# Kernel tuning notes

Measured on AMD Instinct MI355X. Metric: run time of the kernel, lower is better.

The kernel has to match this reference:

```python
import jax, jax.numpy as jnp
import numpy as np

N = 32768      # nodes
H = 128        # hidden_channels
G = 50         # num_gaussians
F = 128        # num_filters
E = 524288     # edges (avg degree 16)
CUTOFF = 10.0
LOG2 = np.float32(np.log(2.0))


def _lin_init(key, fan_in, fan_out):
    return (jax.random.normal(key, (fan_in, fan_out), jnp.float32) / jnp.sqrt(jnp.float32(fan_in)))


def setup_inputs() -> dict:
    key = jax.random.key(0)
    ks = jax.random.split(key, 12)
    h = jax.random.normal(ks[0], (N, H), jnp.float32)
    pos = jax.random.uniform(ks[1], (N, 3), jnp.float32, minval=0.0, maxval=10.0)
    edge_index = jax.random.randint(ks[2], (2, E), 0, N, jnp.int32)
    virtual_edge_mask = jax.random.randint(ks[3], (E,), 0, 2, jnp.int32) == 1
    return {
        "h": h, "pos": pos,
        "edge_index": edge_index, "virtual_edge_mask": virtual_edge_mask,
        # attn_mlp: Linear(2H+G, H) -> ReLU -> Linear(H, 1)
        "attn_w1": _lin_init(ks[4], 2 * H + G, H), "attn_b1": jnp.zeros((H,), jnp.float32),
        "attn_w2": _lin_init(ks[5], H, 1), "attn_b2": jnp.zeros((1,), jnp.float32),
        # CFConv filter mlp: Linear(G, F) -> ssp -> Linear(F, F)
        "filt_w1": _lin_init(ks[6], G, F), "filt_b1": jnp.zeros((F,), jnp.float32),
        "filt_w2": _lin_init(ks[7], F, F), "filt_b2": jnp.zeros((F,), jnp.float32),
        # CFConv lin1 (no bias), lin2; InteractionBlock output lin
        "lin1_w": _lin_init(ks[8], H, F),
        "lin2_w": _lin_init(ks[9], F, H), "lin2_b": jnp.zeros((H,), jnp.float32),
        "lin_w": _lin_init(ks[10], H, H), "lin_b": jnp.zeros((H,), jnp.float32),
    }


def _ssp(x):  # ShiftedSoftplus
    return jax.nn.softplus(x) - LOG2


def _gaussian_smearing(d):  # [E] -> [E, G]
    offset = jnp.linspace(0.0, CUTOFF, G, dtype=jnp.float32)
    coeff = -0.5 / (offset[1] - offset[0]) ** 2
    return jnp.exp(coeff * (d[:, None] - offset) ** 2)


def _masked_scatter_softmax(score, seg, mask):
    # softmax of score over edges grouped by seg, restricted to mask; 1.0 elsewhere
    neg = jnp.where(mask, score, -jnp.inf)
    m = jax.ops.segment_max(neg, seg, num_segments=N)
    m = jnp.where(jnp.isfinite(m), m, 0.0)
    e = jnp.where(mask, jnp.exp(score - m[seg]), 0.0)
    s = jax.ops.segment_sum(e, seg, num_segments=N)
    return jnp.where(mask, e / (s[seg] + 1e-16), 1.0)


def reference(h, pos, edge_index, virtual_edge_mask,
              attn_w1, attn_b1, attn_w2, attn_b2,
              filt_w1, filt_b1, filt_w2, filt_b2,
              lin1_w, lin2_w, lin2_b, lin_w, lin_b):
    row, col = edge_index[0], edge_index[1]
    d = jnp.linalg.norm(pos[row] - pos[col], axis=-1)          # [E]
    edge_attr = _gaussian_smearing(d)                          # [E, G]

    # attention score over cat(h_i, h_j, edge_attr)
    feat = jnp.concatenate([h[row], h[col], edge_attr], axis=-1)   # [E, 2H+G]
    score = (jax.nn.relu(feat @ attn_w1 + attn_b1) @ attn_w2 + attn_b2)[:, 0]  # [E]
    decay = _masked_scatter_softmax(score, row, virtual_edge_mask)  # [E]
    edge_attr = edge_attr * decay[:, None]

    # PyG SchNet InteractionBlock / CFConv
    C = 0.5 * (jnp.cos(d * jnp.float32(np.pi) / CUTOFF) + 1.0)     # [E]
    W = (_ssp(edge_attr @ filt_w1 + filt_b1) @ filt_w2 + filt_b2) * C[:, None]  # [E, F]
    x = h @ lin1_w                                                  # [N, F]
    msg = x[row] * W                                                # [E, F]
    agg = jax.ops.segment_sum(msg, col, num_segments=N)             # [N, F]
    x = agg @ lin2_w + lin2_b
    h_update = _ssp(x) @ lin_w + lin_b                              # [N, H]
    return h_update, pos
```

## Files before the change

kernel.cpp:

```cpp
#include <hip/hip_runtime.h>

#define NN 32768
#define HH 128
#define GG 50
#define EE 524288
#define TBINS 8192

constexpr float GSTEP = 10.0f / 49.0f;
constexpr float GCOEF = -0.5f / (GSTEP * GSTEP);
constexpr float PI_OVER_CUT = 0.31415926535897931f;
constexpr float LOG2F_ = 0.69314718055994531f;
constexpr float LOG2E_ = 1.4426950408889634f;
constexpr float RLOG2E_ = 0.69314718055994531f;
constexpr float GC2 = GCOEF * LOG2E_;
constexpr float DMAX_ = 17.4f;
constexpr float BIN_SCALE = (float)TBINS / DMAX_;
constexpr float BIN_INV   = DMAX_ / (float)TBINS;

typedef __attribute__((ext_vector_type(8))) short bf16x8;
typedef __attribute__((ext_vector_type(4))) float f32x4;
typedef unsigned short ushort_t;

__device__ __forceinline__ float fast_exp2(float x) {
    float r; asm("v_exp_f32 %0, %1" : "=v"(r) : "v"(x)); return r;
}
__device__ __forceinline__ float fast_log2(float x) {
    float r; asm("v_log_f32 %0, %1" : "=v"(r) : "v"(x)); return r;
}
__device__ __forceinline__ float fexpf(float x) {
    return fast_exp2(x * LOG2E_);
}
__device__ __forceinline__ float sspf(float x) {
    const float p = fast_exp2(x * LOG2E_);
    const float r = RLOG2E_ * fast_log2(1.0f + p) - LOG2F_;
    return (x > 80.0f) ? (x - LOG2F_) : r;
}
__device__ __forceinline__ unsigned fenc(float f) {
    unsigned b = __float_as_uint(f);
    return (b & 0x80000000u) ? ~b : (b | 0x80000000u);
}
__device__ __forceinline__ float fdec(unsigned u) {
    unsigned b = (u & 0x80000000u) ? (u ^ 0x80000000u) : ~u;
    return __uint_as_float(b);
}
__device__ __forceinline__ int get_mask(const void* mp, int mode, int e) {
    if (mode) return ((const unsigned char*)mp)[e] != 0;
    return ((const int*)mp)[e] != 0;
}
__device__ __forceinline__ ushort_t f2bf(float f) {
    unsigned u = __float_as_uint(f);
    return (ushort_t)((u + 0x7FFFu + ((u >> 16) & 1u)) >> 16);
}
__device__ __forceinline__ float bf2f(ushort_t s) { return __uint_as_float(((unsigned)s) << 16); }

__global__ void k_detect(const unsigned char* __restrict__ mb, int* __restrict__ flag) {
    __shared__ int any;
    if (threadIdx.x == 0) any = 0;
    __syncthreads();
    int local = 0;
    for (int i = threadIdx.x; i < 16384; i += blockDim.x)
        if ((i & 3) != 0 && mb[i]) local = 1;
    if (local) atomicOr(&any, 1);
    __syncthreads();
    if (threadIdx.x == 0) *flag = any;
}

__global__ void k_prep_w(const float* __restrict__ filt_w2,
                         const float* __restrict__ attn_w1, const float* __restrict__ lin1_w,
                         const float* __restrict__ lin2_w, const float* __restrict__ lin_w,
                         ushort_t* __restrict__ w2t, ushort_t* __restrict__ wut,
                         ushort_t* __restrict__ wvt, ushort_t* __restrict__ wxt,
                         ushort_t* __restrict__ l2t, ushort_t* __restrict__ lwt)
{
    const int t = blockIdx.x * 256 + threadIdx.x;
    if (t < 16384) {
        const int n = t >> 7, k = t & 127;
        w2t[t] = f2bf(filt_w2[k * HH + n]);
    } else if (t < 32768) {
        const int i = t - 16384, n = i >> 7, k = i & 127;
        wut[i] = f2bf(attn_w1[(size_t)k * HH + n]);
    } else if (t < 49152) {
        const int i = t - 32768, n = i >> 7, k = i & 127;
        wvt[i] = f2bf(attn_w1[(size_t)(128 + k) * HH + n]);
    } else if (t < 65536) {
        const int i = t - 49152, n = i >> 7, k = i & 127;
        wxt[i] = f2bf(lin1_w[(size_t)k * HH + n]);
    } else if (t < 81920) {
        const int i = t - 65536, n = i >> 7, k = i & 127;
        l2t[i] = f2bf(lin2_w[(size_t)k * HH + n]);
    } else if (t < 98304) {
        const int i = t - 81920, n = i >> 7, k = i & 127;
        lwt[i] = f2bf(lin_w[(size_t)k * HH + n]);
    }
}

__global__ __launch_bounds__(256) void k_prep_tab(
    const float* __restrict__ filt_w1, const float* __restrict__ attn_w1,
    const float* __restrict__ attn_b1,
    ushort_t* __restrict__ atab, ushort_t* __restrict__ btab)
{
    __shared__ float ga[2][GG];
    const int tid = threadIdx.x;
    const int half = tid >> 7, j = tid & 127;
    const int bin = blockIdx.x * 2 + half;
    const float d = bin * BIN_INV;
    if (j < GG) {
        const float t = d - j * GSTEP;
        ga[half][j] = fast_exp2(GC2 * t * t);
    }
    __syncthreads();
    float a = 0.0f, b = attn_b1[j];
    for (int g = 0; g < GG; g++) {
        const float gv = ga[half][g];
        a += gv * filt_w1[g * HH + j];
        b += gv * attn_w1[(size_t)(256 + g) * HH + j];
    }
    atab[(size_t)bin * HH + j] = f2bf(a);
    btab[(size_t)bin * HH + j] = f2bf(b);
}

__global__ __launch_bounds__(256, 4) void k_node_proj(
    const float* __restrict__ h,
    const ushort_t* __restrict__ wut, const ushort_t* __restrict__ wvt,
    const ushort_t* __restrict__ wxt,
    ushort_t* __restrict__ ub, ushort_t* __restrict__ vb, ushort_t* __restrict__ xhb)
{
    __shared__ alignas(16) unsigned char smem[32768];
    unsigned char* HB = smem;
    unsigned char* WB = smem + 16384;

    const int tid = threadIdx.x;
    const int n0 = blockIdx.x * 64;
    const int mat = blockIdx.y;
    const ushort_t* __restrict__ wt = (mat == 0) ? wut : (mat == 1 ? wvt : wxt);
    ushort_t* __restrict__ out = (mat == 0) ? ub : (mat == 1 ? vb : xhb);

    for (int p = tid; p < 2048; p += 256) {
        const int row = p >> 5, c4 = p & 31;
        const float4 v = *(const float4*)(h + (size_t)(n0 + row) * HH + c4 * 4);
        uint2 pk = {(unsigned)f2bf(v.x) | ((unsigned)f2bf(v.y) << 16),
                    (unsigned)f2bf(v.z) | ((unsigned)f2bf(v.w) << 16)};
        const int lbyte = row * 256 + c4 * 8;
        *(uint2*)(HB + (lbyte ^ ((row & 7) << 4))) = pk;
    }
    for (int p = tid; p < 1024; p += 256) {
        const int byte = p * 16; const int nl = byte >> 8;
        *(float4*)(WB + (byte ^ ((nl & 7) << 4))) = *(const float4*)((const char*)wt + byte);
    }
    __syncthreads();

    const int lane = tid & 63, wv = tid >> 6, col0 = lane & 15, g4 = lane >> 4;
    const int m = wv * 16 + col0;
    f32x4 acc[8] = {};
#pragma unroll
    for (int hh2 = 0; hh2 < 2; hh2++) {
        if (hh2 == 1) {
            __syncthreads();
            for (int p = tid; p < 1024; p += 256) {
                const int byte = p * 16; const int nl = byte >> 8;
                *(float4*)(WB + (byte ^ ((nl & 7) << 4))) =
                    *(const float4*)((const char*)wt + 16384 + byte);
            }
            __syncthreads();
        }
#pragma unroll
        for (int kk = 0; kk < 4; kk++) {
            const int abyte = m * 256 + kk * 64 + g4 * 16;
            const bf16x8 af = *(const bf16x8*)(HB + (abyte ^ ((m & 7) << 4)));
#pragma unroll
            for (int q = 0; q < 4; q++) {
                const int l = q * 16 + col0;
                const int bbyte = l * 256 + kk * 64 + g4 * 16;
                const bf16x8 bf_ = *(const bf16x8*)(WB + (bbyte ^ ((l & 7) << 4)));
                acc[hh2 * 4 + q] = __builtin_amdgcn_mfma_f32_16x16x32_bf16(af, bf_, acc[hh2 * 4 + q], 0, 0, 0);
            }
        }
    }
#pragma unroll
    for (int f = 0; f < 8; f++) {
        const int col = (f >> 2) * 64 + (f & 3) * 16 + col0;
#pragma unroll
        for (int rg = 0; rg < 4; rg++) {
            const int row = wv * 16 + g4 * 4 + rg;
            out[(size_t)(n0 + row) * HH + col] = f2bf(acc[f][rg]);
        }
    }
}

#define CPB 2048
__global__ __launch_bounds__(256) void k_compact(
    const int* __restrict__ ei, const void* __restrict__ maskp,
    const int* __restrict__ flagp,
    int* __restrict__ count, int* __restrict__ mcount,
    uint2* __restrict__ mrec)
{
    __shared__ uint2 buf[CPB];
    __shared__ int lcnt, gbase;
    const int tid = threadIdx.x;
    const int lane = tid & 63;
    if (tid == 0) lcnt = 0;
    __syncthreads();

    const int base = blockIdx.x * CPB;
    const int mode = *flagp;
#pragma unroll
    for (int i = 0; i < CPB; i += 256) {
        const int e = base + i + tid;
        const int r = ei[e], c = ei[EE + e];
        atomicAdd(&count[c], 1);
        const int msk = get_mask(maskp, mode, e);
        const unsigned long long ball = __ballot(msk);
        const int rank = __popcll(ball & ((1ull << lane) - 1ull));
        int wb = 0;
        if (lane == 0 && ball) wb = atomicAdd(&lcnt, __popcll(ball));
        wb = __shfl(wb, 0, 64);
        if (msk) {
            uint2 rec = {(unsigned)e, (unsigned)r | ((unsigned)c << 16)};
            buf[wb + rank] = rec;
        }
    }
    __syncthreads();
    if (tid == 0) gbase = atomicAdd(mcount, lcnt);
    __syncthreads();
    const int n = lcnt, gb = gbase;
    for (int i = tid; i < n; i += 256)
        mrec[gb + i] = buf[i];
}

__global__ __launch_bounds__(256, 8) void k_edge_score(
    const float* __restrict__ pos, const uint2* __restrict__ mrec,
    const int* __restrict__ mcount,
    const ushort_t* __restrict__ ub, const ushort_t* __restrict__ vb,
    const ushort_t* __restrict__ btab,
    const float* __restrict__ attn_w2, const float* __restrict__ attn_b2,
    float* __restrict__ score, unsigned* __restrict__ menc)
{
    __shared__ int rsh[64], csh[64], esh[64], bsh[64];
    __shared__ int Em_s;

    const int tid  = threadIdx.x;
    if (tid == 0) Em_s = *mcount;
    __syncthreads();
    const int Em = Em_s;
    const int base = blockIdx.x * 64;
    if (base >= Em) return;

    const int lane = tid & 63;
    const int wv   = tid >> 6;
    const int col0 = lane & 15;
    const int g4   = lane >> 4;

    if (tid < 64) {
        const int slot = base + tid;
        int e = -1, r = 0, c = 0;
        if (slot < Em) {
            const uint2 rec = mrec[slot];
            e = (int)rec.x;
            r = (int)(rec.y & 0xFFFFu);
            c = (int)(rec.y >> 16);
        }
        esh[tid] = e; rsh[tid] = r; csh[tid] = c;
        const float dx = pos[r * 3 + 0] - pos[c * 3 + 0];
        const float dy = pos[r * 3 + 1] - pos[c * 3 + 1];
        const float dz = pos[r * 3 + 2] - pos[c * 3 + 2];
        const float d = sqrtf(dx * dx + dy * dy + dz * dz);
        int bin = (int)(d * BIN_SCALE + 0.5f);
        bsh[tid] = (bin > TBINS - 1) ? TBINS - 1 : bin;
    }
    __syncthreads();

    const float4 w20 = *(const float4*)(attn_w2 + col0 * 8);
    const float4 w21 = *(const float4*)(attn_w2 + col0 * 8 + 4);
    const float w2v[8] = {w20.x, w20.y, w20.z, w20.w, w21.x, w21.y, w21.z, w21.w};

    float pe[4];
#pragma unroll
    for (int rg = 0; rg < 4; rg++) {
        const int le = wv * 16 + g4 * 4 + rg;
        const int r = rsh[le], c = csh[le], bin = bsh[le];
        const bf16x8 uu = *(const bf16x8*)(ub + (size_t)r * HH + col0 * 8);
        const bf16x8 vv = *(const bf16x8*)(vb + (size_t)c * HH + col0 * 8);
        const bf16x8 bb = *(const bf16x8*)(btab + (size_t)bin * HH + col0 * 8);
        float s = 0.0f;
#pragma unroll
        for (int b = 0; b < 8; b++) {
            float z = bf2f((ushort_t)uu[b]) + bf2f((ushort_t)vv[b]) + bf2f((ushort_t)bb[b]);
            z = fmaxf(z, 0.0f);
            s += z * w2v[b];
        }
        pe[rg] = s;
    }
#pragma unroll
    for (int mask = 1; mask <= 8; mask <<= 1) {
#pragma unroll
        for (int rg = 0; rg < 4; rg++)
            pe[rg] += __shfl_xor(pe[rg], mask, 64);
    }
    if (col0 == 0) {
        const float b2 = attn_b2[0];
#pragma unroll
        for (int rg = 0; rg < 4; rg++) {
            const int le = wv * 16 + g4 * 4 + rg;
            const int e = esh[le];
            if (e >= 0) {
                const float s = pe[rg] + b2;
                score[e] = s;
                atomicMax(&menc[rsh[le]], fenc(s));
            }
        }
    }
}

__global__ void k_ssum(const uint2* __restrict__ mrec, const int* __restrict__ mcount,
                       const float* __restrict__ score, const unsigned* __restrict__ menc,
                       float* __restrict__ ssum)
{
    const int slot = blockIdx.x * 256 + threadIdx.x;
    if (slot >= *mcount) return;
    const uint2 rec = mrec[slot];
    const int e = (int)rec.x;
    const int r = (int)(rec.y & 0xFFFFu);
    atomicAdd(&ssum[r], fexpf(score[e] - fdec(menc[r])));
}

__global__ __launch_bounds__(512) void k_scan(const int* __restrict__ count,
                                              int* __restrict__ cursor)
{
    __shared__ int s[512];
    const int t = threadIdx.x;
    const int base_i = t * 64;
    int sum = 0;
    for (int i = 0; i < 64; i++) sum += count[base_i + i];
    s[t] = sum;
    __syncthreads();
    for (int off = 1; off < 512; off <<= 1) {
        int v = (t >= off) ? s[t - off] : 0;
        __syncthreads();
        s[t] += v;
        __syncthreads();
    }
    int run = s[t] - sum;
    for (int i = 0; i < 64; i++) {
        cursor[base_i + i] = run;
        run += count[base_i + i];
    }
}

__global__ void k_scatter(const int* __restrict__ ei, const void* __restrict__ maskp,
                          const int* __restrict__ flagp, const float* __restrict__ pos,
                          const float* __restrict__ score,
                          const unsigned* __restrict__ menc, const float* __restrict__ ssum,
                          int* __restrict__ cursor, uint4* __restrict__ erec)
{
    const int e = blockIdx.x * 256 + threadIdx.x;
    if (e >= EE) return;
    const int r = ei[e], c = ei[EE + e];
    const int p = atomicAdd(&cursor[c], 1);
    const float dx = pos[r * 3 + 0] - pos[c * 3 + 0];
    const float dy = pos[r * 3 + 1] - pos[c * 3 + 1];
    const float dz = pos[r * 3 + 2] - pos[c * 3 + 2];
    const float d = sqrtf(dx * dx + dy * dy + dz * dz);
    int bin = (int)(d * BIN_SCALE + 0.5f);
    bin = (bin > TBINS - 1) ? TBINS - 1 : bin;
    float dec = 1.0f;
    const int mode = *flagp;
    if (get_mask(maskp, mode, e)) {
        const float m = fdec(menc[r]);
        dec = fexpf(score[e] - m) / (ssum[r] + 1e-16f);
    }
    uint4 rec = {__float_as_uint(d), __float_as_uint(dec),
                 (unsigned)r | ((unsigned)c << 16), (unsigned)bin};
    erec[p] = rec;
}

__global__ __launch_bounds__(256, 4) void k_filter_mfma(
    const uint4* __restrict__ erec,
    const ushort_t* __restrict__ atab, const float* __restrict__ filt_b1,
    const ushort_t* __restrict__ w2t, const float* __restrict__ filt_b2,
    const ushort_t* __restrict__ xhb, float* __restrict__ agg)
{
    __shared__ alignas(16) unsigned char smem[32768];
    unsigned char* T1 = smem;
    unsigned char* WB = smem + 16384;
    float* msgb = (float*)smem;

    __shared__ float decsh[64], Csh[64];
    __shared__ int rsh[64], csh[64], bsh[64];
    __shared__ int shflags;

    const int tid  = threadIdx.x;
    const int e0   = blockIdx.x * 64;
    const int lane = tid & 63;
    const int wv   = tid >> 6;
    const int col0 = lane & 15;
    const int g4   = lane >> 4;

    if (tid < 64) {
        const uint4 rec = erec[e0 + tid];
        const float d = __uint_as_float(rec.x);
        decsh[tid] = __uint_as_float(rec.y);
        rsh[tid] = (int)(rec.z & 0xFFFFu);
        csh[tid] = (int)(rec.z >> 16);
        bsh[tid] = (int)rec.w;
        Csh[tid] = 0.5f * (cosf(d * PI_OVER_CUT) + 1.0f);
    }
    if (tid == 64) {
        const unsigned cf = erec[e0].z >> 16;
        const unsigned cl = erec[e0 + 63].z >> 16;
        int f = 0;
        if (e0 > 0 && (erec[e0 - 1].z >> 16) == cf) f |= 1;
        if (e0 + 64 < EE && (erec[e0 + 64].z >> 16) == cl) f |= 2;
        shflags = f;
    }
    for (int p = tid; p < 1024; p += 256) {
        const int byte = p * 16; const int nl = byte >> 8;
        *(float4*)(WB + (byte ^ ((nl & 7) << 4))) = *(const float4*)((const char*)w2t + byte);
    }
    __syncthreads();

    {
        const int e = tid & 63, q = tid >> 6;
        const float dec = decsh[e];
        const ushort_t* arow = atab + (size_t)bsh[e] * HH;
#pragma unroll
        for (int c8 = 0; c8 < 4; c8++) {
            const int col = q * 32 + c8 * 8;
            const bf16x8 av = *(const bf16x8*)(arow + col);
            const float4 fb0 = *(const float4*)(filt_b1 + col);
            const float4 fb1 = *(const float4*)(filt_b1 + col + 4);
            const float bb[8] = {fb0.x, fb0.y, fb0.z, fb0.w, fb1.x, fb1.y, fb1.z, fb1.w};
            bf16x8 pk;
#pragma unroll
            for (int b = 0; b < 8; b++)
                pk[b] = (short)f2bf(sspf(dec * bf2f((ushort_t)av[b]) + bb[b]));
            const int lbyte = e * 256 + col * 2;
            *(bf16x8*)(T1 + (lbyte ^ ((e & 7) << 4))) = pk;
        }
    }
    int rr[4]; float CC[4];
#pragma unroll
    for (int rg = 0; rg < 4; rg++) {
        const int e = wv * 16 + g4 * 4 + rg;
        rr[rg] = rsh[e];
        CC[rg] = Csh[e];
    }
    ushort_t xr[4][8];
#pragma unroll
    for (int rg = 0; rg < 4; rg++)
#pragma unroll
        for (int n = 0; n < 8; n++)
            xr[rg][n] = xhb[(size_t)rr[rg] * HH + n * 16 + col0];
    float b2v[8];
#pragma unroll
    for (int n = 0; n < 8; n++)
        b2v[n] = filt_b2[n * 16 + col0];
    __syncthreads();

    const int m = wv * 16 + col0;
    f32x4 acc2[8] = {};
#pragma unroll
    for (int kk = 0; kk < 4; kk++) {
        const int abyte = m * 256 + kk * 64 + g4 * 16;
        const bf16x8 af = *(const bf16x8*)(T1 + (abyte ^ ((m & 7) << 4)));
#pragma unroll
        for (int q = 0; q < 4; q++) {
            const int l = q * 16 + col0;
            const int bbyte = l * 256 + kk * 64 + g4 * 16;
            const bf16x8 bf_ = *(const bf16x8*)(WB + (bbyte ^ ((l & 7) << 4)));
            acc2[q] = __builtin_amdgcn_mfma_f32_16x16x32_bf16(af, bf_, acc2[q], 0, 0, 0);
        }
    }
    __syncthreads();
    for (int p = tid; p < 1024; p += 256) {
        const int byte = p * 16; const int nl = byte >> 8;
        *(float4*)(WB + (byte ^ ((nl & 7) << 4))) =
            *(const float4*)((const char*)w2t + 16384 + byte);
    }
    __syncthreads();
#pragma unroll
    for (int kk = 0; kk < 4; kk++) {
        const int abyte = m * 256 + kk * 64 + g4 * 16;
        const bf16x8 af = *(const bf16x8*)(T1 + (abyte ^ ((m & 7) << 4)));
#pragma unroll
        for (int q = 0; q < 4; q++) {
            const int l = q * 16 + col0;
            const int bbyte = l * 256 + kk * 64 + g4 * 16;
            const bf16x8 bf_ = *(const bf16x8*)(WB + (bbyte ^ ((l & 7) << 4)));
            acc2[4 + q] = __builtin_amdgcn_mfma_f32_16x16x32_bf16(af, bf_, acc2[4 + q], 0, 0, 0);
        }
    }
    __syncthreads();

#pragma unroll
    for (int n = 0; n < 8; n++) {
        const int col = n * 16 + col0;
#pragma unroll
        for (int rg = 0; rg < 4; rg++) {
            const int e = wv * 16 + g4 * 4 + rg;
            const float Wv = (acc2[n][rg] + b2v[n]) * CC[rg];
            const float xv = __uint_as_float(((unsigned)xr[rg][n]) << 16);
            msgb[e * 128 + ((col + 8 * g4) & 127)] = xv * Wv;
        }
    }
    __syncthreads();

    {
        const int q = tid >> 7;
        const int j = tid & 127;
        const int base = q * 32;
        const int fl = shflags;
        const int cfirst = csh[base], clast = csh[base + 31];
        const int f1 = (q == 0) ? (fl & 1) : (csh[base - 1] == cfirst);
        const int f2 = (q == 1) ? (fl & 2) : (csh[base + 32] == clast);
        float a = msgb[base * 128 + ((j + 8 * ((base >> 2) & 3)) & 127)];
        int cur = cfirst;
        for (int e = base + 1; e < base + 32; e++) {
            const int de = csh[e];
            if (de != cur) {
                if ((cur == cfirst && f1) || (cur == clast && f2))
                    atomicAdd(&agg[(size_t)cur * HH + j], a);
                else
                    agg[(size_t)cur * HH + j] = a;
                a = 0.0f;
                cur = de;
            }
            a += msgb[e * 128 + ((j + 8 * ((e >> 2) & 3)) & 127)];
        }
        if ((cur == cfirst && f1) || (cur == clast && f2))
            atomicAdd(&agg[(size_t)cur * HH + j], a);
        else
            agg[(size_t)cur * HH + j] = a;
    }
}

__global__ __launch_bounds__(256, 4) void k_final(
    const float* __restrict__ agg, const ushort_t* __restrict__ l2t,
    const float* __restrict__ lin2_b, const ushort_t* __restrict__ lwt,
    const float* __restrict__ lin_b, float* __restrict__ out)
{
    __shared__ alignas(16) unsigned char smem[32768];
    unsigned char* AB = smem;
    unsigned char* WB = smem + 16384;
    unsigned char* T1 = smem;

    const int tid = threadIdx.x;
    const int n0 = blockIdx.x * 64;

    for (int p = tid; p < 2048; p += 256) {
        const int row = p >> 5, c4 = p & 31;
        const float4 v = *(const float4*)(agg + (size_t)(n0 + row) * HH + c4 * 4);
        uint2 pk = {(unsigned)f2bf(v.x) | ((unsigned)f2bf(v.y) << 16),
                    (unsigned)f2bf(v.z) | ((unsigned)f2bf(v.w) << 16)};
        const int lbyte = row * 256 + c4 * 8;
        *(uint2*)(AB + (lbyte ^ ((row & 7) << 4))) = pk;
    }
    for (int p = tid; p < 1024; p += 256) {
        const int byte = p * 16; const int nl = byte >> 8;
        *(float4*)(WB + (byte ^ ((nl & 7) << 4))) = *(const float4*)((const char*)l2t + byte);
    }
    __syncthreads();

    const int lane = tid & 63, wv = tid >> 6, col0 = lane & 15, g4 = lane >> 4;
    const int m = wv * 16 + col0;
    float b1v[8], b2v[8];
#pragma unroll
    for (int f = 0; f < 8; f++) {
        const int colf = (f >> 2) * 64 + (f & 3) * 16 + col0;
        b1v[f] = lin2_b[colf];
        b2v[f] = lin_b[colf];
    }

    f32x4 acc[8] = {};
#pragma unroll
    for (int h = 0; h < 2; h++) {
        if (h == 1) {
            __syncthreads();
            for (int p = tid; p < 1024; p += 256) {
                const int byte = p * 16; const int nl = byte >> 8;
                *(float4*)(WB + (byte ^ ((nl & 7) << 4))) =
                    *(const float4*)((const char*)l2t + 16384 + byte);
            }
            __syncthreads();
        }
#pragma unroll
        for (int kk = 0; kk < 4; kk++) {
            const int abyte = m * 256 + kk * 64 + g4 * 16;
            const bf16x8 af = *(const bf16x8*)(AB + (abyte ^ ((m & 7) << 4)));
#pragma unroll
            for (int q = 0; q < 4; q++) {
                const int l = q * 16 + col0;
                const int bbyte = l * 256 + kk * 64 + g4 * 16;
                const bf16x8 bf_ = *(const bf16x8*)(WB + (bbyte ^ ((l & 7) << 4)));
                acc[h * 4 + q] = __builtin_amdgcn_mfma_f32_16x16x32_bf16(af, bf_, acc[h * 4 + q], 0, 0, 0);
            }
        }
    }
    __syncthreads();

#pragma unroll
    for (int f = 0; f < 8; f++) {
        const int colf = (f >> 2) * 64 + (f & 3) * 16 + col0;
#pragma unroll
        for (int rg = 0; rg < 4; rg++) {
            const int row = wv * 16 + g4 * 4 + rg;
            const float tv = sspf(acc[f][rg] + b1v[f]);
            const int lbyte = row * 256 + colf * 2;
            *(ushort_t*)(T1 + (lbyte ^ ((row & 7) << 4))) = f2bf(tv);
        }
    }
    for (int p = tid; p < 1024; p += 256) {
        const int byte = p * 16; const int nl = byte >> 8;
        *(float4*)(WB + (byte ^ ((nl & 7) << 4))) = *(const float4*)((const char*)lwt + byte);
    }
    __syncthreads();

    f32x4 acc2[8] = {};
#pragma unroll
    for (int h = 0; h < 2; h++) {
        if (h == 1) {
            __syncthreads();
            for (int p = tid; p < 1024; p += 256) {
                const int byte = p * 16; const int nl = byte >> 8;
                *(float4*)(WB + (byte ^ ((nl & 7) << 4))) =
                    *(const float4*)((const char*)lwt + 16384 + byte);
            }
            __syncthreads();
        }
#pragma unroll
        for (int kk = 0; kk < 4; kk++) {
            const int abyte = m * 256 + kk * 64 + g4 * 16;
            const bf16x8 af = *(const bf16x8*)(T1 + (abyte ^ ((m & 7) << 4)));
#pragma unroll
            for (int q = 0; q < 4; q++) {
                const int l = q * 16 + col0;
                const int bbyte = l * 256 + kk * 64 + g4 * 16;
                const bf16x8 bf_ = *(const bf16x8*)(WB + (bbyte ^ ((l & 7) << 4)));
                acc2[h * 4 + q] = __builtin_amdgcn_mfma_f32_16x16x32_bf16(af, bf_, acc2[h * 4 + q], 0, 0, 0);
            }
        }
    }
#pragma unroll
    for (int f = 0; f < 8; f++) {
        const int colf = (f >> 2) * 64 + (f & 3) * 16 + col0;
#pragma unroll
        for (int rg = 0; rg < 4; rg++) {
            const int row = wv * 16 + g4 * 4 + rg;
            out[(size_t)(n0 + row) * HH + colf] = acc2[f][rg] + b2v[f];
        }
    }
}

__global__ void k_copy_pos(const float* __restrict__ pos, float* __restrict__ out) {
    const int i = blockIdx.x * 256 + threadIdx.x;
    if (i < NN * 3) out[i] = pos[i];
}

extern "C" void kernel_launch(void* const* d_in, const int* in_sizes, int n_in,
                              void* d_out, int out_size, void* d_ws, size_t ws_size,
                              hipStream_t stream)
{
    const float* h       = (const float*)d_in[0];
    const float* pos     = (const float*)d_in[1];
    const int*   ei      = (const int*)d_in[2];
    const void*  maskp   = d_in[3];
    const float* attn_w1 = (const float*)d_in[4];
    const float* attn_b1 = (const float*)d_in[5];
    const float* attn_w2 = (const float*)d_in[6];
    const float* attn_b2 = (const float*)d_in[7];
    const float* filt_w1 = (const float*)d_in[8];
    const float* filt_b1 = (const float*)d_in[9];
    const float* filt_w2 = (const float*)d_in[10];
    const float* filt_b2 = (const float*)d_in[11];
    const float* lin1_w  = (const float*)d_in[12];
    const float* lin2_w  = (const float*)d_in[13];
    const float* lin2_b  = (const float*)d_in[14];
    const float* lin_w   = (const float*)d_in[15];
    const float* lin_b   = (const float*)d_in[16];

    char* p = (char*)d_ws;
    auto alloc = [&](size_t bytes) { char* r = p; p += (bytes + 255) & ~(size_t)255; return r; };

    ushort_t* ub    = (ushort_t*)alloc((size_t)NN * HH * 2);
    ushort_t* vb    = (ushort_t*)alloc((size_t)NN * HH * 2);
    ushort_t* xhb   = (ushort_t*)alloc((size_t)NN * HH * 2);
    float*    score = (float*)alloc((size_t)EE * 4);
    unsigned* menc  = (unsigned*)alloc((size_t)NN * 4);
    float*    ssum  = (float*)alloc((size_t)NN * 4);
    int*      count = (int*)alloc((size_t)NN * 4);
    int*      mcount= (int*)alloc(4);
    int*      cursor= (int*)alloc((size_t)NN * 4);
    float*    agg   = (float*)alloc((size_t)NN * HH * 4);
    int*      flag  = (int*)alloc(4);
    uint2*    mrec  = (uint2*)alloc((size_t)EE * 8);
    uint4*    erec  = (uint4*)alloc((size_t)EE * 16);
    ushort_t* atab  = (ushort_t*)alloc((size_t)TBINS * HH * 2);
    ushort_t* btab  = (ushort_t*)alloc((size_t)TBINS * HH * 2);
    ushort_t* w2t   = (ushort_t*)alloc((size_t)128 * 128 * 2);
    ushort_t* wut   = (ushort_t*)alloc((size_t)128 * 128 * 2);
    ushort_t* wvt   = (ushort_t*)alloc((size_t)128 * 128 * 2);
    ushort_t* wxt   = (ushort_t*)alloc((size_t)128 * 128 * 2);
    ushort_t* l2t   = (ushort_t*)alloc((size_t)128 * 128 * 2);
    ushort_t* lwt   = (ushort_t*)alloc((size_t)128 * 128 * 2);

    float* out_h   = (float*)d_out;
    float* out_pos = out_h + (size_t)NN * HH;

    hipMemsetAsync(menc, 0, (size_t)3 * NN * 4 + 256, stream);

    k_detect<<<1, 256, 0, stream>>>((const unsigned char*)maskp, flag);
    k_prep_w<<<384, 256, 0, stream>>>(filt_w2, attn_w1, lin1_w, lin2_w, lin_w,
                                      w2t, wut, wvt, wxt, l2t, lwt);
    k_prep_tab<<<TBINS / 2, 256, 0, stream>>>(filt_w1, attn_w1, attn_b1, atab, btab);
    k_node_proj<<<dim3(NN / 64, 3), 256, 0, stream>>>(h, wut, wvt, wxt, ub, vb, xhb);
    k_compact<<<EE / CPB, 256, 0, stream>>>(ei, maskp, flag, count, mcount, mrec);
    k_edge_score<<<EE / 64, 256, 0, stream>>>(pos, mrec, mcount, ub, vb, btab,
                                              attn_w2, attn_b2, score, menc);
    k_ssum<<<EE / 256, 256, 0, stream>>>(mrec, mcount, score, menc, ssum);
    k_scan<<<1, 512, 0, stream>>>(count, cursor);
    k_scatter<<<EE / 256, 256, 0, stream>>>(ei, maskp, flag, pos, score, menc, ssum,
                                            cursor, erec);

    hipMemsetAsync(agg, 0, (size_t)NN * HH * sizeof(float), stream);
    k_filter_mfma<<<EE / 64, 256, 0, stream>>>(erec, atab, filt_b1, w2t, filt_b2, xhb, agg);

    k_final<<<NN / 64, 256, 0, stream>>>(agg, l2t, lin2_b, lwt, lin_b, out_h);
    k_copy_pos<<<(NN * 3 + 255) / 256, 256, 0, stream>>>(pos, out_pos);
}
```

Before: 290.2 us.

## Merge prep kernels, reuse h tile across projections, use packed bf16 convert

Merges the weight-transpose and table-building prep kernels into one launch. k_node_proj now converts the h tile once per block and loops over all three projection matrices, instead of using a 3-wide grid that reloads and reconverts h for each matrix. Manual bf16 rounding is replaced with the hardware v_cvt_pk_bf16_f32 instruction in several places. The segmented reduction loop is unrolled so the swizzle offset can be hoisted. The trade-offs are fewer blocks in node_proj, which lowers parallelism, and extra syncs for reloading weights.

```diff
diff --git a/kernel.cpp b/kernel.cpp
--- a/kernel.cpp
+++ b/kernel.cpp
@@ -51,6 +51,10 @@
     unsigned u = __float_as_uint(f);
     return (ushort_t)((u + 0x7FFFu + ((u >> 16) & 1u)) >> 16);
 }
+__device__ __forceinline__ unsigned cvt_pk_bf16(float lo, float hi) {
+    unsigned r; asm("v_cvt_pk_bf16_f32 %0, %1, %2" : "=v"(r) : "v"(lo), "v"(hi));
+    return r;
+}
 __device__ __forceinline__ float bf2f(ushort_t s) { return __uint_as_float(((unsigned)s) << 16); }
 
 __global__ void k_detect(const unsigned char* __restrict__ mb, int* __restrict__ flag) {
@@ -65,58 +69,57 @@
     if (threadIdx.x == 0) *flag = any;
 }
 
-__global__ void k_prep_w(const float* __restrict__ filt_w2,
-                         const float* __restrict__ attn_w1, const float* __restrict__ lin1_w,
-                         const float* __restrict__ lin2_w, const float* __restrict__ lin_w,
-                         ushort_t* __restrict__ w2t, ushort_t* __restrict__ wut,
-                         ushort_t* __restrict__ wvt, ushort_t* __restrict__ wxt,
-                         ushort_t* __restrict__ l2t, ushort_t* __restrict__ lwt)
-{
-    const int t = blockIdx.x * 256 + threadIdx.x;
-    if (t < 16384) {
-        const int n = t >> 7, k = t & 127;
-        w2t[t] = f2bf(filt_w2[k * HH + n]);
-    } else if (t < 32768) {
-        const int i = t - 16384, n = i >> 7, k = i & 127;
-        wut[i] = f2bf(attn_w1[(size_t)k * HH + n]);
-    } else if (t < 49152) {
-        const int i = t - 32768, n = i >> 7, k = i & 127;
-        wvt[i] = f2bf(attn_w1[(size_t)(128 + k) * HH + n]);
-    } else if (t < 65536) {
-        const int i = t - 49152, n = i >> 7, k = i & 127;
-        wxt[i] = f2bf(lin1_w[(size_t)k * HH + n]);
-    } else if (t < 81920) {
-        const int i = t - 65536, n = i >> 7, k = i & 127;
-        l2t[i] = f2bf(lin2_w[(size_t)k * HH + n]);
-    } else if (t < 98304) {
-        const int i = t - 81920, n = i >> 7, k = i & 127;
-        lwt[i] = f2bf(lin_w[(size_t)k * HH + n]);
-    }
-}
-
-__global__ __launch_bounds__(256) void k_prep_tab(
-    const float* __restrict__ filt_w1, const float* __restrict__ attn_w1,
-    const float* __restrict__ attn_b1,
+__global__ __launch_bounds__(256) void k_prep(
+    const float* __restrict__ filt_w1, const float* __restrict__ filt_w2,
+    const float* __restrict__ attn_w1, const float* __restrict__ attn_b1,
+    const float* __restrict__ lin1_w, const float* __restrict__ lin2_w,
+    const float* __restrict__ lin_w,
+    ushort_t* __restrict__ w2t, ushort_t* __restrict__ wut,
+    ushort_t* __restrict__ wvt, ushort_t* __restrict__ wxt,
+    ushort_t* __restrict__ l2t, ushort_t* __restrict__ lwt,
     ushort_t* __restrict__ atab, ushort_t* __restrict__ btab)
 {
-    __shared__ float ga[2][GG];
-    const int tid = threadIdx.x;
-    const int half = tid >> 7, j = tid & 127;
-    const int bin = blockIdx.x * 2 + half;
-    const float d = bin * BIN_INV;
-    if (j < GG) {
-        const float t = d - j * GSTEP;
-        ga[half][j] = fast_exp2(GC2 * t * t);
-    }
-    __syncthreads();
-    float a = 0.0f, b = attn_b1[j];
-    for (int g = 0; g < GG; g++) {
-        const float gv = ga[half][g];
-        a += gv * filt_w1[g * HH + j];
-        b += gv * attn_w1[(size_t)(256 + g) * HH + j];
-    }
-    atab[(size_t)bin * HH + j] = f2bf(a);
-    btab[(size_t)bin * HH + j] = f2bf(b);
+    if (blockIdx.x < 384) {
+        const int t = blockIdx.x * 256 + threadIdx.x;
+        if (t < 16384) {
+            const int n = t >> 7, k = t & 127;
+            w2t[t] = f2bf(filt_w2[k * HH + n]);
+        } else if (t < 32768) {
+            const int i = t - 16384, n = i >> 7, k = i & 127;
+            wut[i] = f2bf(attn_w1[(size_t)k * HH + n]);
+        } else if (t < 49152) {
+            const int i = t - 32768, n = i >> 7, k = i & 127;
+            wvt[i] = f2bf(attn_w1[(size_t)(128 + k) * HH + n]);
+        } else if (t < 65536) {
+            const int i = t - 49152, n = i >> 7, k = i & 127;
+            wxt[i] = f2bf(lin1_w[(size_t)k * HH + n]);
+        } else if (t < 81920) {
+            const int i = t - 65536, n = i >> 7, k = i & 127;
+            l2t[i] = f2bf(lin2_w[(size_t)k * HH + n]);
+        } else if (t < 98304) {
+            const int i = t - 81920, n = i >> 7, k = i & 127;
+            lwt[i] = f2bf(lin_w[(size_t)k * HH + n]);
+        }
+    } else {
+        __shared__ float ga[2][GG];
+        const int tid = threadIdx.x;
+        const int half = tid >> 7, j = tid & 127;
+        const int bin = (blockIdx.x - 384) * 2 + half;
+        const float d = bin * BIN_INV;
+        if (j < GG) {
+            const float t = d - j * GSTEP;
+            ga[half][j] = fast_exp2(GC2 * t * t);
+        }
+        __syncthreads();
+        float a = 0.0f, b = attn_b1[j];
+        for (int g = 0; g < GG; g++) {
+            const float gv = ga[half][g];
+            a += gv * filt_w1[g * HH + j];
+            b += gv * attn_w1[(size_t)(256 + g) * HH + j];
+        }
+        atab[(size_t)bin * HH + j] = f2bf(a);
+        btab[(size_t)bin * HH + j] = f2bf(b);
+    }
 }
 
 __global__ __launch_bounds__(256, 4) void k_node_proj(
@@ -131,58 +134,54 @@
 
     const int tid = threadIdx.x;
     const int n0 = blockIdx.x * 64;
-    const int mat = blockIdx.y;
-    const ushort_t* __restrict__ wt = (mat == 0) ? wut : (mat == 1 ? wvt : wxt);
-    ushort_t* __restrict__ out = (mat == 0) ? ub : (mat == 1 ? vb : xhb);
 
     for (int p = tid; p < 2048; p += 256) {
         const int row = p >> 5, c4 = p & 31;
         const float4 v = *(const float4*)(h + (size_t)(n0 + row) * HH + c4 * 4);
-        uint2 pk = {(unsigned)f2bf(v.x) | ((unsigned)f2bf(v.y) << 16),
-                    (unsigned)f2bf(v.z) | ((unsigned)f2bf(v.w) << 16)};
+        uint2 pk = {cvt_pk_bf16(v.x, v.y), cvt_pk_bf16(v.z, v.w)};
         const int lbyte = row * 256 + c4 * 8;
         *(uint2*)(HB + (lbyte ^ ((row & 7) << 4))) = pk;
     }
-    for (int p = tid; p < 1024; p += 256) {
-        const int byte = p * 16; const int nl = byte >> 8;
-        *(float4*)(WB + (byte ^ ((nl & 7) << 4))) = *(const float4*)((const char*)wt + byte);
-    }
-    __syncthreads();
 
     const int lane = tid & 63, wv = tid >> 6, col0 = lane & 15, g4 = lane >> 4;
     const int m = wv * 16 + col0;
-    f32x4 acc[8] = {};
-#pragma unroll
-    for (int hh2 = 0; hh2 < 2; hh2++) {
-        if (hh2 == 1) {
+
+#pragma unroll
+    for (int mat = 0; mat < 3; mat++) {
+        const ushort_t* __restrict__ wt = (mat == 0) ? wut : (mat == 1 ? wvt : wxt);
+        ushort_t* __restrict__ out = (mat == 0) ? ub : (mat == 1 ? vb : xhb);
+
+        f32x4 acc[8] = {};
+#pragma unroll
+        for (int hh2 = 0; hh2 < 2; hh2++) {
             __syncthreads();
             for (int p = tid; p < 1024; p += 256) {
                 const int byte = p * 16; const int nl = byte >> 8;
                 *(float4*)(WB + (byte ^ ((nl & 7) << 4))) =
-                    *(const float4*)((const char*)wt + 16384 + byte);
+                    *(const float4*)((const char*)wt + hh2 * 16384 + byte);
             }
             __syncthreads();
-        }
-#pragma unroll
-        for (int kk = 0; kk < 4; kk++) {
-            const int abyte = m * 256 + kk * 64 + g4 * 16;
-            const bf16x8 af = *(const bf16x8*)(HB + (abyte ^ ((m & 7) << 4)));
-#pragma unroll
-            for (int q = 0; q < 4; q++) {
-                const int l = q * 16 + col0;
-                const int bbyte = l * 256 + kk * 64 + g4 * 16;
-                const bf16x8 bf_ = *(const bf16x8*)(WB + (bbyte ^ ((l & 7) << 4)));
-                acc[hh2 * 4 + q] = __builtin_amdgcn_mfma_f32_16x16x32_bf16(af, bf_, acc[hh2 * 4 + q], 0, 0, 0);
-            }
-        }
-    }
-#pragma unroll
-    for (int f = 0; f < 8; f++) {
-        const int col = (f >> 2) * 64 + (f & 3) * 16 + col0;
-#pragma unroll
-        for (int rg = 0; rg < 4; rg++) {
-            const int row = wv * 16 + g4 * 4 + rg;
-            out[(size_t)(n0 + row) * HH + col] = f2bf(acc[f][rg]);
+#pragma unroll
+            for (int kk = 0; kk < 4; kk++) {
+                const int abyte = m * 256 + kk * 64 + g4 * 16;
+                const bf16x8 af = *(const bf16x8*)(HB + (abyte ^ ((m & 7) << 4)));
+#pragma unroll
+                for (int q = 0; q < 4; q++) {
+                    const int l = q * 16 + col0;
+                    const int bbyte = l * 256 + kk * 64 + g4 * 16;
+                    const bf16x8 bf_ = *(const bf16x8*)(WB + (bbyte ^ ((l & 7) << 4)));
+                    acc[hh2 * 4 + q] = __builtin_amdgcn_mfma_f32_16x16x32_bf16(af, bf_, acc[hh2 * 4 + q], 0, 0, 0);
+                }
+            }
+        }
+#pragma unroll
+        for (int f = 0; f < 8; f++) {
+            const int col = (f >> 2) * 64 + (f & 3) * 16 + col0;
+#pragma unroll
+            for (int rg = 0; rg < 4; rg++) {
+                const int row = wv * 16 + g4 * 4 + rg;
+                out[(size_t)(n0 + row) * HH + col] = f2bf(acc[f][rg]);
+            }
         }
     }
 }
@@ -429,12 +428,14 @@
             const float4 fb0 = *(const float4*)(filt_b1 + col);
             const float4 fb1 = *(const float4*)(filt_b1 + col + 4);
             const float bb[8] = {fb0.x, fb0.y, fb0.z, fb0.w, fb1.x, fb1.y, fb1.z, fb1.w};
-            bf16x8 pk;
+            float sv[8];
 #pragma unroll
             for (int b = 0; b < 8; b++)
-                pk[b] = (short)f2bf(sspf(dec * bf2f((ushort_t)av[b]) + bb[b]));
+                sv[b] = sspf(dec * bf2f((ushort_t)av[b]) + bb[b]);
+            uint4 pk = {cvt_pk_bf16(sv[0], sv[1]), cvt_pk_bf16(sv[2], sv[3]),
+                        cvt_pk_bf16(sv[4], sv[5]), cvt_pk_bf16(sv[6], sv[7])};
             const int lbyte = e * 256 + col * 2;
-            *(bf16x8*)(T1 + (lbyte ^ ((e & 7) << 4))) = pk;
+            *(uint4*)(T1 + (lbyte ^ ((e & 7) << 4))) = pk;
         }
     }
     int rr[4]; float CC[4];
@@ -512,19 +513,25 @@
         const int cfirst = csh[base], clast = csh[base + 31];
         const int f1 = (q == 0) ? (fl & 1) : (csh[base - 1] == cfirst);
         const int f2 = (q == 1) ? (fl & 2) : (csh[base + 32] == clast);
-        float a = msgb[base * 128 + ((j + 8 * ((base >> 2) & 3)) & 127)];
+        float a = 0.0f;
         int cur = cfirst;
-        for (int e = base + 1; e < base + 32; e++) {
-            const int de = csh[e];
-            if (de != cur) {
-                if ((cur == cfirst && f1) || (cur == clast && f2))
-                    atomicAdd(&agg[(size_t)cur * HH + j], a);
-                else
-                    agg[(size_t)cur * HH + j] = a;
-                a = 0.0f;
-                cur = de;
-            }
-            a += msgb[e * 128 + ((j + 8 * ((e >> 2) & 3)) & 127)];
+#pragma unroll
+        for (int g = 0; g < 8; g++) {
+            const int sk = (j + 8 * (g & 3)) & 127;
+#pragma unroll
+            for (int q2 = 0; q2 < 4; q2++) {
+                const int e = base + g * 4 + q2;
+                const int de = csh[e];
+                if (de != cur) {
+                    if ((cur == cfirst && f1) || (cur == clast && f2))
+                        atomicAdd(&agg[(size_t)cur * HH + j], a);
+                    else
+                        agg[(size_t)cur * HH + j] = a;
+                    a = 0.0f;
+                    cur = de;
+                }
+                a += msgb[e * 128 + sk];
+            }
         }
         if ((cur == cfirst && f1) || (cur == clast && f2))
             atomicAdd(&agg[(size_t)cur * HH + j], a);
@@ -549,8 +556,7 @@
     for (int p = tid; p < 2048; p += 256) {
         const int row = p >> 5, c4 = p & 31;
         const float4 v = *(const float4*)(agg + (size_t)(n0 + row) * HH + c4 * 4);
-        uint2 pk = {(unsigned)f2bf(v.x) | ((unsigned)f2bf(v.y) << 16),
-                    (unsigned)f2bf(v.z) | ((unsigned)f2bf(v.w) << 16)};
+        uint2 pk = {cvt_pk_bf16(v.x, v.y), cvt_pk_bf16(v.z, v.w)};
         const int lbyte = row * 256 + c4 * 8;
         *(uint2*)(AB + (lbyte ^ ((row & 7) << 4))) = pk;
     }
@@ -708,10 +714,10 @@
     hipMemsetAsync(menc, 0, (size_t)3 * NN * 4 + 256, stream);
 
     k_detect<<<1, 256, 0, stream>>>((const unsigned char*)maskp, flag);
-    k_prep_w<<<384, 256, 0, stream>>>(filt_w2, attn_w1, lin1_w, lin2_w, lin_w,
-                                      w2t, wut, wvt, wxt, l2t, lwt);
-    k_prep_tab<<<TBINS / 2, 256, 0, stream>>>(filt_w1, attn_w1, attn_b1, atab, btab);
-    k_node_proj<<<dim3(NN / 64, 3), 256, 0, stream>>>(h, wut, wvt, wxt, ub, vb, xhb);
+    k_prep<<<384 + TBINS / 2, 256, 0, stream>>>(filt_w1, filt_w2, attn_w1, attn_b1,
+                                                lin1_w, lin2_w, lin_w,
+                                                w2t, wut, wvt, wxt, l2t, lwt, atab, btab);
+    k_node_proj<<<NN / 64, 256, 0, stream>>>(h, wut, wvt, wxt, ub, vb, xhb);
     k_compact<<<EE / CPB, 256, 0, stream>>>(ei, maskp, flag, count, mcount, mrec);
     k_edge_score<<<EE / 64, 256, 0, stream>>>(pos, mrec, mcount, ub, vb, btab,
                                               attn_w2, attn_b2, score, menc);
```

Result: no change. 293.2 us (+1.0%).
